# Performance work log

Measured on AMD Instinct MI355X. Metric: run time of the kernel, lower is better.

## Reference

```python
import jax, jax.numpy as jnp
import numpy as np


def _gcn_conv(x, W, b, src, dst, dinv):
    # PyG GCNConv: linear transform, then symmetric-normalized aggregation, then bias
    n = x.shape[0]
    h = x @ W  # [N, out]
    norm = (dinv[src] * dinv[dst])[:, None]  # [E, 1]
    msg = h[src] * norm  # gather + scale, [E, out]
    out = jax.ops.segment_sum(msg, dst, num_segments=n)  # scatter-add
    return out + b


def setup_inputs() -> dict:
    key = jax.random.key(0)
    k1, k2, k3, k4 = jax.random.split(key, 4)
    N, E, F_IN, F_HID, F_OUT = 50000, 800000, 512, 256, 64
    x = jax.random.normal(k1, (N, F_IN), dtype=jnp.float32)
    edge_index = jax.random.randint(k2, (2, E), 0, N, dtype=jnp.int64)
    # Glorot-ish init for weights
    W1 = jax.random.normal(k3, (F_IN, F_HID), dtype=jnp.float32) * (1.0 / np.sqrt(F_IN))
    b1 = jnp.zeros((F_HID,), dtype=jnp.float32)
    W2 = jax.random.normal(k4, (F_HID, F_OUT), dtype=jnp.float32) * (1.0 / np.sqrt(F_HID))
    b2 = jnp.zeros((F_OUT,), dtype=jnp.float32)
    return {"x": x, "edge_index": edge_index, "W1": W1, "b1": b1, "W2": W2, "b2": b2}


def reference(x, edge_index, W1, b1, W2, b2):
    n = x.shape[0]
    # Add self loops (GCNConv default)
    loop = jnp.arange(n, dtype=edge_index.dtype)
    src = jnp.concatenate([edge_index[0], loop])
    dst = jnp.concatenate([edge_index[1], loop])
    # Symmetric normalization D^{-1/2} (A+I) D^{-1/2}
    deg = jax.ops.segment_sum(jnp.ones_like(dst, dtype=x.dtype), dst, num_segments=n)
    dinv = jnp.where(deg > 0, jax.lax.rsqrt(deg), 0.0)
    h = _gcn_conv(x, W1, b1, src, dst, dinv)
    h = jax.nn.relu(h)
    # Dropout(p=0.5) is identity in eval mode (deterministic reference)
    h = _gcn_conv(h, W2, b2, src, dst, dinv)
    return jax.nn.log_softmax(h, axis=1)
```

## Files before the change

### kernel.cpp

```cpp
#include <hip/hip_runtime.h>
#include <math.h>

#define F_IN  512
#define F_HID 256
#define F_OUT 64

typedef __attribute__((ext_vector_type(8))) short bf16x8;
typedef __attribute__((ext_vector_type(4))) short bf16x4;
typedef __attribute__((ext_vector_type(4))) float f32x4;

#define GLOBAL_AS __attribute__((address_space(1)))
#define LDS_AS    __attribute__((address_space(3)))

__device__ __forceinline__ void gload_lds16(const void* g, void* l) {
    __builtin_amdgcn_global_load_lds((const GLOBAL_AS uint32_t*)g,
                                     (LDS_AS uint32_t*)l, 16, 0, 0);
}

__device__ __forceinline__ ushort f2bf(float f) {
    union { float f; uint32_t u; } v; v.f = f;
    uint32_t r = (v.u + 0x7FFFu + ((v.u >> 16) & 1u)) >> 16;
    return (ushort)r;
}

__device__ __forceinline__ float bf2f(ushort u) {
    union { uint32_t u; float f; } v; v.u = ((uint32_t)u) << 16;
    return v.f;
}

__device__ __forceinline__ bf16x8 conv8(float4 a, float4 b) {
    bf16x8 c;
    c[0] = (short)f2bf(a.x); c[1] = (short)f2bf(a.y);
    c[2] = (short)f2bf(a.z); c[3] = (short)f2bf(a.w);
    c[4] = (short)f2bf(b.x); c[5] = (short)f2bf(b.y);
    c[6] = (short)f2bf(b.z); c[7] = (short)f2bf(b.w);
    return c;
}

__global__ __launch_bounds__(256) void k_prep(
        const float* __restrict__ W1, ushort* __restrict__ w1t,
        const float* __restrict__ W2, ushort* __restrict__ w2t,
        int* __restrict__ deg, int N) {
    __shared__ ushort t[32][33];
    int bid = blockIdx.x;
    for (int i = bid * 256 + threadIdx.x; i < N; i += 144 * 256) deg[i] = 0;
    const float* W; ushort* Wt; int K, Nc, tk, tn;
    if (bid < 128) { W = W1; Wt = w1t; K = 512; Nc = 256; tk = bid >> 3; tn = bid & 7; }
    else { int b = bid - 128; W = W2; Wt = w2t; K = 256; Nc = 64; tk = b >> 1; tn = b & 1; }
    int r = threadIdx.x >> 5, c = threadIdx.x & 31;
    #pragma unroll
    for (int l = 0; l < 4; ++l)
        t[r + l * 8][c] = f2bf(W[(size_t)(tk * 32 + r + l * 8) * Nc + tn * 32 + c]);
    __syncthreads();
    #pragma unroll
    for (int l = 0; l < 4; ++l)
        Wt[(size_t)(tn * 32 + r + l * 8) * K + tk * 32 + c] = t[c][r + l * 8];
}

__global__ void k_scan1(const int* __restrict__ deg, int* __restrict__ offs,
                        int* __restrict__ bsums, float* __restrict__ dinv, int N) {
    __shared__ int s[256];
    int tid = threadIdx.x;
    int i = blockIdx.x * 256 + tid;
    int v = (i < N) ? deg[i] : 0;
    if (i < N) dinv[i] = rsqrtf((float)(v + 1));
    s[tid] = v; __syncthreads();
    for (int d = 1; d < 256; d <<= 1) {
        int t = (tid >= d) ? s[tid - d] : 0;
        __syncthreads();
        s[tid] += t;
        __syncthreads();
    }
    if (i < N) offs[i] = s[tid] - v;
    if (tid == 255) bsums[blockIdx.x] = s[255];
}

__global__ void k_scan2(int* __restrict__ bsums, int n) {
    __shared__ int s[256];
    int tid = threadIdx.x;
    int v = (tid < n) ? bsums[tid] : 0;
    s[tid] = v; __syncthreads();
    for (int d = 1; d < 256; d <<= 1) {
        int t = (tid >= d) ? s[tid - d] : 0;
        __syncthreads();
        s[tid] += t;
        __syncthreads();
    }
    if (tid < n) bsums[tid] = s[tid] - v;
}

__global__ void k_scan3(int* __restrict__ offs, const int* __restrict__ bsums,
                        int* __restrict__ cursor, int2* __restrict__ jw, int N, int E) {
    int i = blockIdx.x * 256 + threadIdx.x;
    if (i < N) {
        int o = offs[i] + bsums[i >> 8];
        offs[i] = o;
        cursor[i] = o;
    }
    if (i == 0) offs[N] = E;
    if (i < 32) jw[E + i] = make_int2(0, 0);
}

__global__ void k_fill(const int* __restrict__ src, const int* __restrict__ dst,
                       int* __restrict__ cursor, int2* __restrict__ jw,
                       const float* __restrict__ dinv, int E) {
    int e = blockIdx.x * 256 + threadIdx.x;
    if (e < E) {
        int s = src[e];
        int pos = atomicAdd(&cursor[dst[e]], 1);
        jw[pos] = make_int2(s, __float_as_int(dinv[s]));
    }
}

__global__ __launch_bounds__(256) void k_gemm1(
        const float* __restrict__ A, const ushort* __restrict__ Bt,
        ushort* __restrict__ C, int M, int nyblk,
        const int* __restrict__ dst, int* __restrict__ deg, int E) {
    constexpr int K = F_IN, Nc = F_HID, BM = 64, NT = K / 64;
    constexpr int ASTR = 72;
    __shared__ ushort As[2][BM * ASTR];
    __shared__ ushort Bs[2][128 * 64];
    const int tid  = threadIdx.x;
    const int wave = tid >> 6, lane = tid & 63;
    const int wr = wave & 1, wc = wave >> 1;
    const int l15 = lane & 15, hi = lane >> 4;

    int L = blockIdx.x;
    int nfull = (2 * nyblk) & ~15;
    int bx, by;
    if (L < nfull) { bx = (L >> 3) & 1; by = (L >> 4) * 8 + (L & 7); }
    else { int t = L - nfull; bx = t & 1; by = nfull / 2 + (t >> 1); }
    const int brow = by * BM, bcol = bx * 128;

    f32x4 acc[2][4];
    #pragma unroll
    for (int m = 0; m < 2; ++m)
        #pragma unroll
        for (int n = 0; n < 4; ++n) acc[m][n] = (f32x4){0.f, 0.f, 0.f, 0.f};

    const int arow = tid >> 2;
    const int akc  = (tid & 3) * 16;
    int agrow = brow + arow; if (agrow >= M) agrow = M - 1;
    const float4* ap = (const float4*)&A[(size_t)agrow * K + akc];
    const int bc = (lane & 7) ^ ((lane >> 3) & 7);
    const ushort* bp[4];
    int bdst[4];
    #pragma unroll
    for (int l = 0; l < 4; ++l) {
        int g = l * 4 + wave;
        int R = g * 8 + (lane >> 3);
        bp[l]   = &Bt[(size_t)(bcol + R) * K + bc * 8];
        bdst[l] = g * 512;
    }

    {
        float4 v0 = ap[0], v1 = ap[1], v2 = ap[2], v3 = ap[3];
        *(bf16x8*)&As[0][arow * ASTR + akc]     = conv8(v0, v1);
        *(bf16x8*)&As[0][arow * ASTR + akc + 8] = conv8(v2, v3);
        #pragma unroll
        for (int l = 0; l < 4; ++l) gload_lds16(bp[l], &Bs[0][bdst[l]]);
    }
    __syncthreads();

    #pragma unroll
    for (int t = 0; t < NT; ++t) {
        const int b = t & 1;
        if (t + 1 < NT) {
            #pragma unroll
            for (int l = 0; l < 4; ++l)
                gload_lds16(bp[l] + (t + 1) * 64, &Bs[b ^ 1][bdst[l]]);
            float4 v0 = ap[(t + 1) * 16], v1 = ap[(t + 1) * 16 + 1],
                   v2 = ap[(t + 1) * 16 + 2], v3 = ap[(t + 1) * 16 + 3];
            *(bf16x8*)&As[b ^ 1][arow * ASTR + akc]     = conv8(v0, v1);
            *(bf16x8*)&As[b ^ 1][arow * ASTR + akc + 8] = conv8(v2, v3);
        }
        if (t == 1) {
            int e0 = blockIdx.x * 512 + tid;
            if (e0 < E) atomicAdd(&deg[dst[e0]], 1);
        }
        if (t == 4) {
            int e1 = blockIdx.x * 512 + 256 + tid;
            if (e1 < E) atomicAdd(&deg[dst[e1]], 1);
        }
        #pragma unroll
        for (int ks = 0; ks < 2; ++ks) {
            const int kqA = ks * 32 + hi * 8;
            bf16x8 af[2], bfr[4];
            #pragma unroll
            for (int m = 0; m < 2; ++m)
                af[m] = *(const bf16x8*)&As[b][(wr * 32 + l15 + m * 16) * ASTR + kqA];
            #pragma unroll
            for (int n = 0; n < 4; ++n) {
                const int row = wc * 64 + l15 + n * 16;
                const int p = (ks * 4 + hi) ^ (l15 & 7);
                bfr[n] = *(const bf16x8*)&Bs[b][row * 64 + p * 8];
            }
            #pragma unroll
            for (int m = 0; m < 2; ++m)
                #pragma unroll
                for (int n = 0; n < 4; ++n)
                    acc[m][n] = __builtin_amdgcn_mfma_f32_16x16x32_bf16(af[m], bfr[n], acc[m][n], 0, 0, 0);
        }
        if (t + 1 < NT) __syncthreads();
    }

    const int crow0 = brow + wr * 32 + hi * 4;
    const int ccol0 = bcol + wc * 64 + l15;
    #pragma unroll
    for (int m = 0; m < 2; ++m)
        #pragma unroll
        for (int n = 0; n < 4; ++n)
            #pragma unroll
            for (int j = 0; j < 4; ++j) {
                int row = crow0 + m * 16 + j;
                if (row < M) C[(size_t)row * Nc + ccol0 + n * 16] = f2bf(acc[m][n][j]);
            }
}

template<int WR, int WC, int MR, int NR>
__global__ __launch_bounds__(256) void k_gemm_bf16(
        const ushort* __restrict__ A, const ushort* __restrict__ Bt,
        ushort* __restrict__ C, int M, int K, int Nc) {
    constexpr int BM = WR * MR * 16;
    constexpr int BN = WC * NR * 16;
    __shared__ ushort As[BM * 32];
    __shared__ ushort Bs[BN * 32];
    const int tid  = threadIdx.x;
    const int wave = tid >> 6, lane = tid & 63;
    const int wr = wave % WR, wc = wave / WR;
    const int brow = blockIdx.y * BM, bcol = blockIdx.x * BN;

    f32x4 acc[MR][NR];
    #pragma unroll
    for (int m = 0; m < MR; ++m)
        #pragma unroll
        for (int n = 0; n < NR; ++n) acc[m][n] = (f32x4){0.f, 0.f, 0.f, 0.f};

    const int srow = tid >> 2;
    const int scol = (tid & 3) * 8;
    const int kq  = (lane >> 4) * 8;
    const int rA0 = wr * MR * 16 + (lane & 15);
    const int rB0 = wc * NR * 16 + (lane & 15);

    for (int k0 = 0; k0 < K; k0 += 32) {
        #pragma unroll
        for (int l = 0; l < BM / 64; ++l) {
            int row = brow + l * 64 + srow;
            if (row >= M) row = M - 1;
            gload_lds16(&A[(size_t)row * K + k0 + scol], &As[l * 2048 + wave * 512]);
        }
        #pragma unroll
        for (int l = 0; l < BN / 64; ++l) {
            int row = bcol + l * 64 + srow;
            gload_lds16(&Bt[(size_t)row * K + k0 + scol], &Bs[l * 2048 + wave * 512]);
        }
        __syncthreads();
        bf16x8 af[MR], bfr[NR];
        #pragma unroll
        for (int m = 0; m < MR; ++m)
            af[m] = *(const bf16x8*)&As[(rA0 + m * 16) * 32 + kq];
        #pragma unroll
        for (int n = 0; n < NR; ++n)
            bfr[n] = *(const bf16x8*)&Bs[(rB0 + n * 16) * 32 + kq];
        #pragma unroll
        for (int m = 0; m < MR; ++m)
            #pragma unroll
            for (int n = 0; n < NR; ++n)
                acc[m][n] = __builtin_amdgcn_mfma_f32_16x16x32_bf16(af[m], bfr[n], acc[m][n], 0, 0, 0);
        __syncthreads();
    }

    const int crow0 = brow + wr * MR * 16 + (lane >> 4) * 4;
    const int ccol0 = bcol + wc * NR * 16 + (lane & 15);
    #pragma unroll
    for (int m = 0; m < MR; ++m)
        #pragma unroll
        for (int n = 0; n < NR; ++n)
            #pragma unroll
            for (int j = 0; j < 4; ++j) {
                int row = crow0 + m * 16 + j;
                if (row < M) C[(size_t)row * Nc + ccol0 + n * 16] = f2bf(acc[m][n][j]);
            }
}

__global__ __launch_bounds__(256) void k_agg1(
        const ushort* __restrict__ h, const int2* __restrict__ jw,
        const int* __restrict__ offs, const float* __restrict__ dinv,
        const float* __restrict__ bias, ushort* __restrict__ outm, int N) {
    int wave = threadIdx.x >> 6, lane = threadIdx.x & 63;
    int i = blockIdx.x * 4 + wave;
    if (i >= N) return;
    int g = lane & 31;
    int p = lane >> 5;
    float di = dinv[i];
    float acc[8];
    {
        bf16x8 hv = *(const bf16x8*)&h[(size_t)i * F_HID + g * 8];
        float w = (p == 0) ? di * di : 0.f;
        #pragma unroll
        for (int k = 0; k < 8; ++k) acc[k] = bf2f((ushort)hv[k]) * w;
    }
    int s = offs[i], e = offs[i + 1];
    for (int u = s; u < e; u += 16) {
        int2 a[8];
        #pragma unroll
        for (int q = 0; q < 8; ++q) a[q] = jw[u + 2 * q + p];
        bf16x8 hv[8];
        #pragma unroll
        for (int q = 0; q < 8; ++q)
            hv[q] = *(const bf16x8*)&h[(size_t)a[q].x * F_HID + g * 8];
        #pragma unroll
        for (int q = 0; q < 8; ++q) {
            float ww = (u + 2 * q + p < e) ? __int_as_float(a[q].y) * di : 0.f;
            #pragma unroll
            for (int k = 0; k < 8; ++k) acc[k] += bf2f((ushort)hv[q][k]) * ww;
        }
    }
    #pragma unroll
    for (int k = 0; k < 8; ++k) acc[k] += __shfl_xor(acc[k], 32, 64);
    if (p == 0) {
        float4 b0 = *(const float4*)&bias[g * 8];
        float4 b1 = *(const float4*)&bias[g * 8 + 4];
        bf16x8 o;
        o[0] = (short)f2bf(fmaxf(acc[0] + b0.x, 0.f));
        o[1] = (short)f2bf(fmaxf(acc[1] + b0.y, 0.f));
        o[2] = (short)f2bf(fmaxf(acc[2] + b0.z, 0.f));
        o[3] = (short)f2bf(fmaxf(acc[3] + b0.w, 0.f));
        o[4] = (short)f2bf(fmaxf(acc[4] + b1.x, 0.f));
        o[5] = (short)f2bf(fmaxf(acc[5] + b1.y, 0.f));
        o[6] = (short)f2bf(fmaxf(acc[6] + b1.z, 0.f));
        o[7] = (short)f2bf(fmaxf(acc[7] + b1.w, 0.f));
        *(bf16x8*)&outm[(size_t)i * F_HID + g * 8] = o;
    }
}

__global__ __launch_bounds__(256) void k_agg2(
        const ushort* __restrict__ h, const int2* __restrict__ jw,
        const int* __restrict__ offs, const float* __restrict__ dinv,
        const float* __restrict__ bias, float* __restrict__ outm, int N) {
    int wave = threadIdx.x >> 6, lane = threadIdx.x & 63;
    int i = blockIdx.x * 4 + wave;
    if (i >= N) return;
    int g4 = lane & 15;
    int p  = lane >> 4;
    float di = dinv[i];
    float acc[4];
    {
        bf16x4 hv = *(const bf16x4*)&h[(size_t)i * F_OUT + g4 * 4];
        float w = (p == 0) ? di * di : 0.f;
        #pragma unroll
        for (int k = 0; k < 4; ++k) acc[k] = bf2f((ushort)hv[k]) * w;
    }
    int s = offs[i], e = offs[i + 1];
    for (int u = s; u < e; u += 32) {
        int2 a[8];
        #pragma unroll
        for (int q = 0; q < 8; ++q) a[q] = jw[u + 4 * q + p];
        bf16x4 hv[8];
        #pragma unroll
        for (int q = 0; q < 8; ++q)
            hv[q] = *(const bf16x4*)&h[(size_t)a[q].x * F_OUT + g4 * 4];
        #pragma unroll
        for (int q = 0; q < 8; ++q) {
            float ww = (u + 4 * q + p < e) ? __int_as_float(a[q].y) * di : 0.f;
            #pragma unroll
            for (int k = 0; k < 4; ++k) acc[k] += bf2f((ushort)hv[q][k]) * ww;
        }
    }
    #pragma unroll
    for (int k = 0; k < 4; ++k) {
        acc[k] += __shfl_xor(acc[k], 16, 64);
        acc[k] += __shfl_xor(acc[k], 32, 64);
    }
    float4 bv = *(const float4*)&bias[g4 * 4];
    acc[0] += bv.x; acc[1] += bv.y; acc[2] += bv.z; acc[3] += bv.w;
    float m = fmaxf(fmaxf(acc[0], acc[1]), fmaxf(acc[2], acc[3]));
    #pragma unroll
    for (int o = 8; o >= 1; o >>= 1) m = fmaxf(m, __shfl_xor(m, o, 64));
    float ssum = expf(acc[0] - m) + expf(acc[1] - m) + expf(acc[2] - m) + expf(acc[3] - m);
    #pragma unroll
    for (int o = 8; o >= 1; o >>= 1) ssum += __shfl_xor(ssum, o, 64);
    float lse = m + logf(ssum);
    if (p == 0) {
        float4 o4;
        o4.x = acc[0] - lse; o4.y = acc[1] - lse;
        o4.z = acc[2] - lse; o4.w = acc[3] - lse;
        *(float4*)&outm[(size_t)i * F_OUT + g4 * 4] = o4;
    }
}

extern "C" void kernel_launch(void* const* d_in, const int* in_sizes, int n_in,
                              void* d_out, int out_size, void* d_ws, size_t ws_size,
                              hipStream_t stream) {
    const float* x  = (const float*)d_in[0];
    const int*   ei = (const int*)d_in[1];
    const float* W1 = (const float*)d_in[2];
    const float* b1 = (const float*)d_in[3];
    const float* W2 = (const float*)d_in[4];
    const float* b2 = (const float*)d_in[5];
    float* out = (float*)d_out;

    int N = in_sizes[0] / F_IN;
    int E = in_sizes[1] / 2;
    const int* src = ei;
    const int* dst = ei + E;

    ushort* w1t = (ushort*)d_ws;
    ushort* w2t = w1t + F_HID * F_IN;
    ushort* h1  = w2t + F_OUT * F_HID;
    ushort* a1  = h1 + (size_t)N * F_HID;
    int*    deg = (int*)(a1 + (size_t)N * F_HID);
    float*  dinv = (float*)(deg + N);
    int*    offs = (int*)(dinv + N);
    int*    cursor = offs + N + 1;
    int*    bsums  = cursor + N;
    int2*   jw = (int2*)(((uintptr_t)(bsums + 256) + 7) & ~(uintptr_t)7);
    ushort* h2 = h1;

    int nch = (N + 255) / 256;
    int nyblk = (N + 63) / 64;

    k_prep<<<144, 256, 0, stream>>>(W1, w1t, W2, w2t, deg, N);

    k_gemm1<<<2 * nyblk, 256, 0, stream>>>(x, w1t, h1, N, nyblk, dst, deg, E);

    k_scan1<<<nch, 256, 0, stream>>>(deg, offs, bsums, dinv, N);
    k_scan2<<<1, 256, 0, stream>>>(bsums, nch);
    k_scan3<<<nch, 256, 0, stream>>>(offs, bsums, cursor, jw, N, E);
    k_fill<<<(E + 255) / 256, 256, 0, stream>>>(src, dst, cursor, jw, dinv, E);

    k_agg1<<<(N + 3) / 4, 256, 0, stream>>>(h1, jw, offs, dinv, b1, a1, N);

    k_gemm_bf16<4, 1, 1, 4><<<dim3(1, (N + 63) / 64), 256, 0, stream>>>(
        a1, w2t, h2, N, F_HID, F_OUT);

    k_agg2<<<(N + 3) / 4, 256, 0, stream>>>(h2, jw, offs, dinv, b2, out, N);
}
```

Baseline: 225.4 us.

## Split layer-1 aggregation into 8 feature slabs per node with wider edge parallelism

```diff
diff --git a/kernel.cpp b/kernel.cpp
--- a/kernel.cpp
+++ b/kernel.cpp
@@ -98,7 +98,7 @@
         cursor[i] = o;
     }
     if (i == 0) offs[N] = E;
-    if (i < 32) jw[E + i] = make_int2(0, 0);
+    if (i < 64) jw[E + i] = make_int2(0, 0);
 }
 
 __global__ void k_fill(const int* __restrict__ src, const int* __restrict__ dst,
@@ -288,49 +288,50 @@
         const int* __restrict__ offs, const float* __restrict__ dinv,
         const float* __restrict__ bias, ushort* __restrict__ outm, int N) {
     int wave = threadIdx.x >> 6, lane = threadIdx.x & 63;
-    int i = blockIdx.x * 4 + wave;
+    int slab = blockIdx.x & 7;
+    int i = (blockIdx.x >> 3) * 4 + wave;
     if (i >= N) return;
-    int g = lane & 31;
-    int p = lane >> 5;
+    int g = lane & 7;
+    int p = lane >> 3;
+    int fb = slab * 32 + g * 4;
     float di = dinv[i];
-    float acc[8];
+    float acc[4];
     {
-        bf16x8 hv = *(const bf16x8*)&h[(size_t)i * F_HID + g * 8];
+        bf16x4 hv = *(const bf16x4*)&h[(size_t)i * F_HID + fb];
         float w = (p == 0) ? di * di : 0.f;
         #pragma unroll
-        for (int k = 0; k < 8; ++k) acc[k] = bf2f((ushort)hv[k]) * w;
-    }
-    int s = offs[i], e = offs[i + 1];
-    for (int u = s; u < e; u += 16) {
+        for (int k = 0; k < 4; ++k) acc[k] = bf2f((ushort)hv[k]) * w;
+    }
+    int s0 = offs[i], e = offs[i + 1];
+    for (int u = s0; u < e; u += 64) {
         int2 a[8];
         #pragma unroll
-        for (int q = 0; q < 8; ++q) a[q] = jw[u + 2 * q + p];
-        bf16x8 hv[8];
+        for (int q = 0; q < 8; ++q) a[q] = jw[u + 8 * q + p];
+        bf16x4 hv[8];
         #pragma unroll
         for (int q = 0; q < 8; ++q)
-            hv[q] = *(const bf16x8*)&h[(size_t)a[q].x * F_HID + g * 8];
+            hv[q] = *(const bf16x4*)&h[(size_t)a[q].x * F_HID + fb];
         #pragma unroll
         for (int q = 0; q < 8; ++q) {
-            float ww = (u + 2 * q + p < e) ? __int_as_float(a[q].y) * di : 0.f;
-            #pragma unroll
-            for (int k = 0; k < 8; ++k) acc[k] += bf2f((ushort)hv[q][k]) * ww;
-        }
-    }
-    #pragma unroll
-    for (int k = 0; k < 8; ++k) acc[k] += __shfl_xor(acc[k], 32, 64);
+            float ww = (u + 8 * q + p < e) ? __int_as_float(a[q].y) * di : 0.f;
+            #pragma unroll
+            for (int k = 0; k < 4; ++k) acc[k] += bf2f((ushort)hv[q][k]) * ww;
+        }
+    }
+    #pragma unroll
+    for (int k = 0; k < 4; ++k) {
+        acc[k] += __shfl_xor(acc[k], 8, 64);
+        acc[k] += __shfl_xor(acc[k], 16, 64);
+        acc[k] += __shfl_xor(acc[k], 32, 64);
+    }
     if (p == 0) {
-        float4 b0 = *(const float4*)&bias[g * 8];
-        float4 b1 = *(const float4*)&bias[g * 8 + 4];
-        bf16x8 o;
-        o[0] = (short)f2bf(fmaxf(acc[0] + b0.x, 0.f));
-        o[1] = (short)f2bf(fmaxf(acc[1] + b0.y, 0.f));
-        o[2] = (short)f2bf(fmaxf(acc[2] + b0.z, 0.f));
-        o[3] = (short)f2bf(fmaxf(acc[3] + b0.w, 0.f));
-        o[4] = (short)f2bf(fmaxf(acc[4] + b1.x, 0.f));
-        o[5] = (short)f2bf(fmaxf(acc[5] + b1.y, 0.f));
-        o[6] = (short)f2bf(fmaxf(acc[6] + b1.z, 0.f));
-        o[7] = (short)f2bf(fmaxf(acc[7] + b1.w, 0.f));
-        *(bf16x8*)&outm[(size_t)i * F_HID + g * 8] = o;
+        float4 bv = *(const float4*)&bias[fb];
+        bf16x4 o;
+        o[0] = (short)f2bf(fmaxf(acc[0] + bv.x, 0.f));
+        o[1] = (short)f2bf(fmaxf(acc[1] + bv.y, 0.f));
+        o[2] = (short)f2bf(fmaxf(acc[2] + bv.z, 0.f));
+        o[3] = (short)f2bf(fmaxf(acc[3] + bv.w, 0.f));
+        *(bf16x4*)&outm[(size_t)i * F_HID + fb] = o;
     }
 }
 
@@ -429,7 +430,7 @@
     k_scan3<<<nch, 256, 0, stream>>>(offs, bsums, cursor, jw, N, E);
     k_fill<<<(E + 255) / 256, 256, 0, stream>>>(src, dst, cursor, jw, dinv, E);
 
-    k_agg1<<<(N + 3) / 4, 256, 0, stream>>>(h1, jw, offs, dinv, b1, a1, N);
+    k_agg1<<<((N + 3) / 4) * 8, 256, 0, stream>>>(h1, jw, offs, dinv, b1, a1, N);
 
     k_gemm_bf16<4, 1, 1, 4><<<dim3(1, (N + 63) / 64), 256, 0, stream>>>(
         a1, w2t, h2, N, F_HID, F_OUT);
```

Result: slower. 400.4 us (+77.6%).
